# Performance work log

Hardware: AMD Instinct MI355X
Metric: run time of the kernel (lower is better)

Reference implementation:

```python
import jax, jax.numpy as jnp
import numpy as np

B, C, H, W = 4, 256, 64, 64
D, K = 256, 32
EPS = 1e-12  # F.normalize clamp

def setup_inputs() -> dict:
    key = jax.random.key(0)
    k1, k2, k3, k4 = jax.random.split(key, 4)
    x = jax.random.normal(k1, (B, C, H, W), dtype=jnp.float32)
    w_theta = jax.random.normal(k2, (D, C), dtype=jnp.float32) * 0.05  # 1x1 conv theta
    w_phi = jax.random.normal(k3, (K, C // K), dtype=jnp.float32) * 0.1  # grouped 1x1 conv phi
    scale = jax.random.uniform(k4, (D, K), dtype=jnp.float32, minval=-1.0, maxval=0.0)
    return {"x": x, "w_theta": w_theta, "w_phi": w_phi, "scale": scale}

def reference(x, w_theta, w_phi, scale):
    b, c, h, w = x.shape
    d, k = scale.shape
    n = h * w
    xf = x.reshape(b, c, n)                                   # B,D,N (C==D)
    # --- Gen_code ---
    xg = xf.reshape(b, k, c // k, n)                          # grouped 1x1 conv
    x_phi = jnp.einsum('bkcn,kc->bnk', xg, w_phi)             # B,N,K
    x_phi = jax.nn.softmax(x_phi, axis=1)                     # softmax over pixels
    x_theta = jnp.einsum('dc,bcn->bdn', w_theta, xf)          # B,D,N
    code = jnp.einsum('bdn,bnk->bdk', x_theta, x_phi)         # B,D,K
    code = code / jnp.maximum(jnp.linalg.norm(code, axis=1, keepdims=True), EPS)
    # (dropout p=0.15 treated as identity)
    # --- embedded residual, without materializing B,N,D,K ---
    s2 = scale * scale                                        # D,K
    t1 = jnp.einsum('bdn,dk->bnk', xf * xf, s2)
    t2 = jnp.einsum('bdn,bdk->bnk', xf, s2[None] * code)
    t3 = jnp.einsum('dk,bdk->bk', s2, code * code)
    dist = t1 - 2.0 * t2 + t3[:, None, :]                     # sum_d (scale*(x-code))^2
    Q = jax.nn.softmax(-0.5 * dist, axis=2)                   # B,N,K
    Qsum = Q.sum(axis=1)                                      # B,K
    # Z_[b,d,k] = sum_n Q*residual / Qsum = scale*(sum_n Q x / Qsum - code)
    Z_ = scale[None] * (jnp.einsum('bdn,bnk->bdk', xf, Q) / Qsum[:, None, :] - code)
    Z = Z_ / jnp.sqrt((Z_ * Z_).sum(axis=1, keepdims=True))   # torch sqrt, no eps
    return Z, Q
```

## Files before the change

### kernel.cpp

```cpp
#include <hip/hip_runtime.h>
#include <math.h>

#define BB 4
#define CC 256
#define NN 4096
#define KK 32
#define DD 256
#define GG 8
#define NT2 64
#define NE 8

__device__ __forceinline__ float wredsum(float v) {
#pragma unroll
  for (int o = 32; o > 0; o >>= 1) v += __shfl_xor(v, o, 64);
  return v;
}

__global__ __launch_bounds__(256) void k_phi(const float* __restrict__ x,
                                             const float* __restrict__ wphi,
                                             float* __restrict__ phi,
                                             float* __restrict__ Sp) {
  const int half = blockIdx.x & 1;
  const int k = (blockIdx.x >> 1) & 31;
  const int b = blockIdx.x >> 6;
  const int tid = threadIdx.x;
  const float* xb = x + (size_t)(b * CC + k * GG) * NN + half * 2048;
  float w[GG];
#pragma unroll
  for (int j = 0; j < GG; ++j) w[j] = wphi[k * GG + j];
  float4 v[2];
  float sum = 0.f;
#pragma unroll
  for (int i = 0; i < 2; ++i) {
    const int n = i * 1024 + tid * 4;
    float4 s = make_float4(0.f, 0.f, 0.f, 0.f);
#pragma unroll
    for (int j = 0; j < GG; ++j) {
      const float4 xv = *reinterpret_cast<const float4*>(xb + (size_t)j * NN + n);
      s.x = fmaf(xv.x, w[j], s.x);
      s.y = fmaf(xv.y, w[j], s.y);
      s.z = fmaf(xv.z, w[j], s.z);
      s.w = fmaf(xv.w, w[j], s.w);
    }
    v[i].x = __expf(s.x);
    v[i].y = __expf(s.y);
    v[i].z = __expf(s.z);
    v[i].w = __expf(s.w);
    sum += v[i].x + v[i].y + v[i].z + v[i].w;
  }
  float* pk = phi + (size_t)(b * KK + k) * NN + half * 2048;
#pragma unroll
  for (int i = 0; i < 2; ++i) {
    *reinterpret_cast<float4*>(pk + i * 1024 + tid * 4) = v[i];
  }
  __shared__ float rb[4];
  sum = wredsum(sum);
  if ((tid & 63) == 0) rb[tid >> 6] = sum;
  __syncthreads();
  if (tid == 0)
    Sp[((size_t)half * BB + b) * KK + k] = rb[0] + rb[1] + rb[2] + rb[3];
}

__global__ __launch_bounds__(256) void k_xpT(const float* __restrict__ x,
                                             const float* __restrict__ phi,
                                             float* __restrict__ m1e) {
  const int e = blockIdx.x & 7;
  const int ct = (blockIdx.x >> 3) & 31;
  const int b = blockIdx.x >> 8;
  const int tid = threadIdx.x;
  __shared__ float smem[256 * 33];
  const int kl = tid >> 3;
  const int nq = tid & 7;
  const int k = tid & 31;
  const int g = tid >> 5;
  const float* xb = x + (size_t)(b * CC + ct * 8) * NN + e * 512;
  float acc[8] = {0.f, 0.f, 0.f, 0.f, 0.f, 0.f, 0.f, 0.f};
#pragma unroll
  for (int ch = 0; ch < 2; ++ch) {
    const float* pch = phi + (size_t)(b * KK + kl) * NN + e * 512 + ch * 256;
#pragma unroll
    for (int j = 0; j < 8; ++j) {
      const int nn = (j * 8 + nq) * 4;
      const float4 pv = *reinterpret_cast<const float4*>(pch + nn);
      smem[(nn + 0) * 33 + kl] = pv.x;
      smem[(nn + 1) * 33 + kl] = pv.y;
      smem[(nn + 2) * 33 + kl] = pv.z;
      smem[(nn + 3) * 33 + kl] = pv.w;
    }
    __syncthreads();
#pragma unroll
    for (int i = 0; i < 8; ++i) {
      const int nl = g * 32 + i * 4;
      const float p0 = smem[(nl + 0) * 33 + k];
      const float p1 = smem[(nl + 1) * 33 + k];
      const float p2 = smem[(nl + 2) * 33 + k];
      const float p3 = smem[(nl + 3) * 33 + k];
#pragma unroll
      for (int c = 0; c < 8; ++c) {
        const float4 xv =
            *reinterpret_cast<const float4*>(xb + (size_t)c * NN + ch * 256 + nl);
        acc[c] = fmaf(xv.x, p0, acc[c]);
        acc[c] = fmaf(xv.y, p1, acc[c]);
        acc[c] = fmaf(xv.z, p2, acc[c]);
        acc[c] = fmaf(xv.w, p3, acc[c]);
      }
    }
    __syncthreads();
  }
#pragma unroll
  for (int c = 0; c < 8; ++c) smem[(g * 8 + c) * 33 + k] = acc[c];
  __syncthreads();
  const int c2 = tid & 7, k2 = tid >> 3;
  float s = 0.f;
#pragma unroll
  for (int gg = 0; gg < 8; ++gg) s += smem[(gg * 8 + c2) * 33 + k2];
  m1e[((size_t)(e * BB + b) * KK + k2) * CC + ct * 8 + c2] = s;
}

__global__ __launch_bounds__(256) void k_code(const float* __restrict__ m1e,
                                              const float* __restrict__ Sp,
                                              const float* __restrict__ wth,
                                              const float* __restrict__ scale,
                                              float* __restrict__ code,
                                              float* __restrict__ bc2,
                                              float* __restrict__ s2g,
                                              float* __restrict__ t3) {
  const int b = blockIdx.x >> 5;
  const int k = blockIdx.x & 31;
  const int d = threadIdx.x;
  const float invS =
      1.f / (Sp[(size_t)b * KK + k] + Sp[((size_t)BB + b) * KK + k]);
  __shared__ __align__(16) float m1s[CC];
  float m = 0.f;
#pragma unroll
  for (int e = 0; e < NE; ++e)
    m += m1e[((size_t)(e * BB + b) * KK + k) * CC + d];
  m1s[d] = m * invS;
  __syncthreads();
  float cd = 0.f;
  const float* wt = wth + (size_t)d * CC;
#pragma unroll 4
  for (int c = 0; c < CC; c += 4) {
    const float4 w4 = *reinterpret_cast<const float4*>(wt + c);
    const float4 m4 = *reinterpret_cast<const float4*>(&m1s[c]);
    cd = fmaf(w4.x, m4.x, cd);
    cd = fmaf(w4.y, m4.y, cd);
    cd = fmaf(w4.z, m4.z, cd);
    cd = fmaf(w4.w, m4.w, cd);
  }
  __shared__ float rb[4];
  float ss = wredsum(cd * cd);
  if ((d & 63) == 0) rb[d >> 6] = ss;
  __syncthreads();
  const float nrm = sqrtf(rb[0] + rb[1] + rb[2] + rb[3]);
  const float inv = 1.f / fmaxf(nrm, 1e-12f);
  cd *= inv;
  const float sc = scale[(size_t)d * KK + k];
  const float s2 = sc * sc;
  code[((size_t)b * DD + d) * KK + k] = cd;
  bc2[((size_t)b * DD + d) * KK + k] = 2.f * s2 * cd;
  if (b == 0) s2g[(size_t)d * KK + k] = s2;
  float tt = wredsum(s2 * cd * cd);
  __syncthreads();
  if ((d & 63) == 0) rb[d >> 6] = tt;
  __syncthreads();
  if (d == 0) t3[b * KK + k] = rb[0] + rb[1] + rb[2] + rb[3];
}

__global__ __launch_bounds__(512) void k_dist(const float* __restrict__ x,
                                              const float* __restrict__ s2g,
                                              const float* __restrict__ bc2,
                                              const float* __restrict__ t3,
                                              float* __restrict__ qout,
                                              float* __restrict__ qpart) {
  const int b = blockIdx.x >> 6;
  const int tile = blockIdx.x & 63;
  const int n0 = tile * 64;
  const int tid = threadIdx.x;
  const int lane = tid & 63;
  const int wid = __builtin_amdgcn_readfirstlane(tid >> 6);
  const int d0 = wid * 32;
  __shared__ float lds[4 * 64 * 33];
  __shared__ float smax[64 * 9];
  __shared__ float ssum[64 * 9];
  float accA[32], accB[32];
#pragma unroll
  for (int k = 0; k < 32; ++k) { accA[k] = 0.f; accB[k] = 0.f; }
  const float* xb = x + ((size_t)b * CC + d0) * NN + n0 + lane;
  const float* s2b = s2g + (size_t)d0 * KK;
  const float* bcb = bc2 + ((size_t)b * DD + d0) * KK;
#pragma unroll 2
  for (int dd = 0; dd < 32; ++dd) {
    const float xv = xb[(size_t)dd * NN];
    const float x2 = xv * xv;
    const float* s2r = s2b + dd * KK;
    const float* bcr = bcb + dd * KK;
#pragma unroll
    for (int k = 0; k < 32; ++k) {
      accA[k] = fmaf(x2, s2r[k], accA[k]);
      accB[k] = fmaf(xv, bcr[k], accB[k]);
    }
  }
  if (wid >= 4) {
    float* Lp = lds + ((size_t)((wid - 4) * 64 + lane)) * 33;
#pragma unroll
    for (int k = 0; k < 32; ++k) Lp[k] = accA[k] - accB[k];
  }
  __syncthreads();
  if (wid < 4) {
    float* Lp = lds + ((size_t)(wid * 64 + lane)) * 33;
#pragma unroll
    for (int k = 0; k < 32; ++k) Lp[k] += accA[k] - accB[k];
  }
  __syncthreads();
  const int n = lane;
  const int kq = wid;
  float vals[4];
#pragma unroll
  for (int j = 0; j < 4; ++j) {
    const int k = kq * 4 + j;
    float s = 0.f;
#pragma unroll
    for (int g = 0; g < 4; ++g) s += lds[((size_t)(g * 64 + n)) * 33 + k];
    vals[j] = -0.5f * (s + t3[b * KK + k]);
  }
  float m4 = fmaxf(fmaxf(vals[0], vals[1]), fmaxf(vals[2], vals[3]));
  smax[n * 9 + kq] = m4;
  __syncthreads();
  float m = smax[n * 9 + 0];
#pragma unroll
  for (int g = 1; g < 8; ++g) m = fmaxf(m, smax[n * 9 + g]);
  float e[4];
  float ps = 0.f;
#pragma unroll
  for (int j = 0; j < 4; ++j) {
    e[j] = __expf(vals[j] - m);
    ps += e[j];
  }
  ssum[n * 9 + kq] = ps;
  __syncthreads();
  float tot = 0.f;
#pragma unroll
  for (int g = 0; g < 8; ++g) tot += ssum[n * 9 + g];
  const float inv = 1.f / tot;
  float4 q4;
  q4.x = e[0] * inv; q4.y = e[1] * inv; q4.z = e[2] * inv; q4.w = e[3] * inv;
  *reinterpret_cast<float4*>(qout + ((size_t)b * NN + n0 + n) * KK + kq * 4) = q4;
  float qs[4] = {q4.x, q4.y, q4.z, q4.w};
#pragma unroll
  for (int j = 0; j < 4; ++j) {
    const float v = wredsum(qs[j]);
    if (n == 0) qpart[((size_t)b * KK + kq * 4 + j) * NT2 + tile] = v;
  }
}

__global__ __launch_bounds__(256) void k_xq(const float* __restrict__ x,
                                            const float* __restrict__ q,
                                            float* __restrict__ znq8) {
  const int e = blockIdx.x & 7;
  const int ct = (blockIdx.x >> 3) & 31;
  const int b = blockIdx.x >> 8;
  const int tid = threadIdx.x;
  const int k = tid & 31;
  const int g = tid >> 5;
  const int n0 = e * 512 + g * 64;
  const float* xb = x + (size_t)(b * CC + ct * 8) * NN;
  const float* qb = q + (size_t)b * NN * KK + k;
  float acc[8] = {0.f, 0.f, 0.f, 0.f, 0.f, 0.f, 0.f, 0.f};
  for (int n = n0; n < n0 + 64; n += 4) {
    const float p0 = qb[(size_t)(n + 0) * KK];
    const float p1 = qb[(size_t)(n + 1) * KK];
    const float p2 = qb[(size_t)(n + 2) * KK];
    const float p3 = qb[(size_t)(n + 3) * KK];
#pragma unroll
    for (int c = 0; c < 8; ++c) {
      const float4 xv = *reinterpret_cast<const float4*>(xb + (size_t)c * NN + n);
      acc[c] = fmaf(xv.x, p0, acc[c]);
      acc[c] = fmaf(xv.y, p1, acc[c]);
      acc[c] = fmaf(xv.z, p2, acc[c]);
      acc[c] = fmaf(xv.w, p3, acc[c]);
    }
  }
  __shared__ float lds[8 * 8 * 33];
#pragma unroll
  for (int c = 0; c < 8; ++c) lds[(g * 8 + c) * 33 + k] = acc[c];
  __syncthreads();
  const int c2 = tid & 7, k2 = tid >> 3;
  float s = 0.f;
#pragma unroll
  for (int gg = 0; gg < 8; ++gg) s += lds[(gg * 8 + c2) * 33 + k2];
  znq8[((size_t)(e * BB + b) * KK + k2) * CC + ct * 8 + c2] = s;
}

__global__ __launch_bounds__(256) void k_z(const float* __restrict__ znq8,
                                           const float* __restrict__ code,
                                           const float* __restrict__ scale,
                                           const float* __restrict__ qpart,
                                           float* __restrict__ zout) {
  const int b = blockIdx.x >> 5;
  const int k = blockIdx.x & 31;
  const int d = threadIdx.x;
  __shared__ float rb[4];
  float qp = 0.f;
  if (d < NT2) qp = qpart[((size_t)b * KK + k) * NT2 + d];
  qp = wredsum(qp);
  if ((d & 63) == 0) rb[d >> 6] = qp;
  __syncthreads();
  const float qs = rb[0] + rb[1] + rb[2] + rb[3];
  float zn = 0.f;
#pragma unroll
  for (int e = 0; e < NE; ++e)
    zn += znq8[((size_t)(e * BB + b) * KK + k) * CC + d];
  const float cd = code[((size_t)b * DD + d) * KK + k];
  const float z_ = scale[(size_t)d * KK + k] * (zn / qs - cd);
  float ss = wredsum(z_ * z_);
  __syncthreads();
  if ((d & 63) == 0) rb[d >> 6] = ss;
  __syncthreads();
  const float rn = 1.f / sqrtf(rb[0] + rb[1] + rb[2] + rb[3]);
  zout[((size_t)b * DD + d) * KK + k] = z_ * rn;
}

extern "C" void kernel_launch(void* const* d_in, const int* in_sizes, int n_in,
                              void* d_out, int out_size, void* d_ws, size_t ws_size,
                              hipStream_t stream) {
  const float* x = (const float*)d_in[0];
  const float* wth = (const float*)d_in[1];
  const float* wphi = (const float*)d_in[2];
  const float* scale = (const float*)d_in[3];
  float* out = (float*)d_out;
  float* zout = out;
  float* qout = out + (size_t)BB * DD * KK;
  float* ws = (float*)d_ws;
  float* phi = ws;
  float* Sp = phi + (size_t)BB * NN * KK;
  float* m1e = Sp + 2 * (size_t)BB * KK;
  float* code = m1e + (size_t)NE * BB * KK * CC;
  float* bc2 = code + (size_t)BB * DD * KK;
  float* s2g = bc2 + (size_t)BB * DD * KK;
  float* t3 = s2g + (size_t)DD * KK;
  float* qpart = t3 + BB * KK;
  float* znq8 = qpart + (size_t)BB * KK * NT2;

  k_phi<<<BB * KK * 2, 256, 0, stream>>>(x, wphi, phi, Sp);
  k_xpT<<<BB * 32 * NE, 256, 0, stream>>>(x, phi, m1e);
  k_code<<<BB * KK, 256, 0, stream>>>(m1e, Sp, wth, scale, code, bc2, s2g, t3);
  k_dist<<<BB * NT2, 512, 0, stream>>>(x, s2g, bc2, t3, qout, qpart);
  k_xq<<<BB * 32 * NE, 256, 0, stream>>>(x, qout, znq8);
  k_z<<<BB * KK, 256, 0, stream>>>(znq8, code, scale, qpart, zout);
}
```

Measured before the change: 78.03 us.

## Fuse six kernels into one cooperative kernel with grid-wide syncs

```diff
diff --git a/kernel.cpp b/kernel.cpp
--- a/kernel.cpp
+++ b/kernel.cpp
@@ -1,5 +1,8 @@
 #include <hip/hip_runtime.h>
+#include <hip/hip_cooperative_groups.h>
 #include <math.h>
+
+namespace cg = cooperative_groups;
 
 #define BB 4
 #define CC 256
@@ -16,314 +19,356 @@
   return v;
 }
 
-__global__ __launch_bounds__(256) void k_phi(const float* __restrict__ x,
-                                             const float* __restrict__ wphi,
-                                             float* __restrict__ phi,
-                                             float* __restrict__ Sp) {
-  const int half = blockIdx.x & 1;
-  const int k = (blockIdx.x >> 1) & 31;
-  const int b = blockIdx.x >> 6;
+__global__ __launch_bounds__(512) void k_mega(
+    const float* __restrict__ x, const float* __restrict__ wth,
+    const float* __restrict__ wphi, const float* __restrict__ scale,
+    float* __restrict__ zout, float* __restrict__ qout,
+    float* __restrict__ phi, float* __restrict__ Sp, float* __restrict__ m1e,
+    float* __restrict__ code, float* __restrict__ bc2, float* __restrict__ s2g,
+    float* __restrict__ t3, float* __restrict__ qpart,
+    float* __restrict__ znq8) {
+  cg::grid_group grid = cg::this_grid();
+  const int bid = blockIdx.x;
   const int tid = threadIdx.x;
-  const float* xb = x + (size_t)(b * CC + k * GG) * NN + half * 2048;
-  float w[GG];
-#pragma unroll
-  for (int j = 0; j < GG; ++j) w[j] = wphi[k * GG + j];
-  float4 v[2];
-  float sum = 0.f;
-#pragma unroll
-  for (int i = 0; i < 2; ++i) {
-    const int n = i * 1024 + tid * 4;
+  __shared__ float smem[9600];
+  __shared__ float rb[8];
+
+  {
+    const int half = bid & 1, k = (bid >> 1) & 31, b = bid >> 6;
+    const int n = half * 2048 + tid * 4;
+    const float* xb = x + (size_t)(b * CC + k * GG) * NN + n;
+    float w[GG];
+#pragma unroll
+    for (int j = 0; j < GG; ++j) w[j] = wphi[k * GG + j];
     float4 s = make_float4(0.f, 0.f, 0.f, 0.f);
 #pragma unroll
     for (int j = 0; j < GG; ++j) {
-      const float4 xv = *reinterpret_cast<const float4*>(xb + (size_t)j * NN + n);
+      const float4 xv = *reinterpret_cast<const float4*>(xb + (size_t)j * NN);
       s.x = fmaf(xv.x, w[j], s.x);
       s.y = fmaf(xv.y, w[j], s.y);
       s.z = fmaf(xv.z, w[j], s.z);
       s.w = fmaf(xv.w, w[j], s.w);
     }
-    v[i].x = __expf(s.x);
-    v[i].y = __expf(s.y);
-    v[i].z = __expf(s.z);
-    v[i].w = __expf(s.w);
-    sum += v[i].x + v[i].y + v[i].z + v[i].w;
-  }
-  float* pk = phi + (size_t)(b * KK + k) * NN + half * 2048;
-#pragma unroll
-  for (int i = 0; i < 2; ++i) {
-    *reinterpret_cast<float4*>(pk + i * 1024 + tid * 4) = v[i];
-  }
-  __shared__ float rb[4];
-  sum = wredsum(sum);
-  if ((tid & 63) == 0) rb[tid >> 6] = sum;
-  __syncthreads();
-  if (tid == 0)
-    Sp[((size_t)half * BB + b) * KK + k] = rb[0] + rb[1] + rb[2] + rb[3];
+    float4 e4;
+    e4.x = __expf(s.x); e4.y = __expf(s.y);
+    e4.z = __expf(s.z); e4.w = __expf(s.w);
+    *reinterpret_cast<float4*>(phi + (size_t)(b * KK + k) * NN + n) = e4;
+    float sum = wredsum(e4.x + e4.y + e4.z + e4.w);
+    if ((tid & 63) == 0) rb[tid >> 6] = sum;
+    __syncthreads();
+    if (tid == 0) {
+      float t = 0.f;
+#pragma unroll
+      for (int i = 0; i < 8; ++i) t += rb[i];
+      Sp[((size_t)half * BB + b) * KK + k] = t;
+    }
+  }
+  grid.sync();
+
+  {
+    const int b = bid >> 6, e = (bid >> 3) & 7, ct = bid & 7;
+    const int k = tid & 31, g = tid >> 5;
+    const int kl = tid >> 4, nq = tid & 15;
+    float acc[32];
+#pragma unroll
+    for (int c = 0; c < 32; ++c) acc[c] = 0.f;
+    const int ne0 = e * 512;
+    const float* xbase = x + (size_t)(b * CC + ct * 32) * NN;
+#pragma unroll
+    for (int ch = 0; ch < 2; ++ch) {
+      const int n0 = ne0 + ch * 256;
+      const float* pk = phi + (size_t)(b * KK + kl) * NN + n0 + nq * 16;
+#pragma unroll
+      for (int j = 0; j < 4; ++j) {
+        const float4 pv = *reinterpret_cast<const float4*>(pk + j * 4);
+        const int nn = nq * 16 + j * 4;
+        smem[(nn + 0) * 33 + kl] = pv.x;
+        smem[(nn + 1) * 33 + kl] = pv.y;
+        smem[(nn + 2) * 33 + kl] = pv.z;
+        smem[(nn + 3) * 33 + kl] = pv.w;
+      }
+      __syncthreads();
+      float ph[16];
+#pragma unroll
+      for (int i = 0; i < 16; ++i) ph[i] = smem[(g * 16 + i) * 33 + k];
+#pragma unroll
+      for (int c = 0; c < 32; ++c) {
+        const float* xr = xbase + (size_t)c * NN + n0 + g * 16;
+#pragma unroll
+        for (int j = 0; j < 4; ++j) {
+          const float4 xv = *reinterpret_cast<const float4*>(xr + j * 4);
+          acc[c] = fmaf(xv.x, ph[j * 4 + 0], acc[c]);
+          acc[c] = fmaf(xv.y, ph[j * 4 + 1], acc[c]);
+          acc[c] = fmaf(xv.z, ph[j * 4 + 2], acc[c]);
+          acc[c] = fmaf(xv.w, ph[j * 4 + 3], acc[c]);
+        }
+      }
+      __syncthreads();
+    }
+    if (g >= 8) {
+#pragma unroll
+      for (int c = 0; c < 32; ++c) smem[((g - 8) * 32 + c) * 33 + k] = acc[c];
+    }
+    __syncthreads();
+    if (g < 8) {
+#pragma unroll
+      for (int c = 0; c < 32; ++c) smem[(g * 32 + c) * 33 + k] += acc[c];
+    }
+    __syncthreads();
+#pragma unroll
+    for (int o = 0; o < 2; ++o) {
+      const int idx = o * 512 + tid;
+      const int c2 = idx >> 5, k2 = idx & 31;
+      float s = 0.f;
+#pragma unroll
+      for (int gg = 0; gg < 8; ++gg) s += smem[(gg * 32 + c2) * 33 + k2];
+      m1e[((size_t)(e * BB + b) * KK + k2) * CC + ct * 32 + c2] = s;
+    }
+  }
+  grid.sync();
+
+  {
+    const bool blkact = bid < 128;
+    const int b = (bid >> 5) & 3, k = bid & 31;
+    const bool act = blkact && (tid < 256);
+    const int d = tid;
+    if (act) {
+      const float invS =
+          1.f / (Sp[(size_t)b * KK + k] + Sp[((size_t)BB + b) * KK + k]);
+      float m = 0.f;
+#pragma unroll
+      for (int e = 0; e < NE; ++e)
+        m += m1e[((size_t)(e * BB + b) * KK + k) * CC + d];
+      smem[d] = m * invS;
+    }
+    __syncthreads();
+    float cd = 0.f;
+    if (act) {
+      const float* wt = wth + (size_t)d * CC;
+#pragma unroll 4
+      for (int c = 0; c < CC; c += 4) {
+        const float4 w4 = *reinterpret_cast<const float4*>(wt + c);
+        cd = fmaf(w4.x, smem[c + 0], cd);
+        cd = fmaf(w4.y, smem[c + 1], cd);
+        cd = fmaf(w4.z, smem[c + 2], cd);
+        cd = fmaf(w4.w, smem[c + 3], cd);
+      }
+    }
+    float ss = wredsum(act ? cd * cd : 0.f);
+    if ((tid & 63) == 0) rb[tid >> 6] = ss;
+    __syncthreads();
+    float nr2 = 0.f;
+#pragma unroll
+    for (int i = 0; i < 8; ++i) nr2 += rb[i];
+    const float inv = 1.f / fmaxf(sqrtf(nr2), 1e-12f);
+    float tt = 0.f;
+    if (act) {
+      cd *= inv;
+      const float sc = scale[(size_t)d * KK + k];
+      const float s2 = sc * sc;
+      code[((size_t)b * DD + d) * KK + k] = cd;
+      bc2[((size_t)b * DD + d) * KK + k] = 2.f * s2 * cd;
+      if (b == 0) s2g[(size_t)d * KK + k] = s2;
+      tt = s2 * cd * cd;
+    }
+    float t2 = wredsum(tt);
+    __syncthreads();
+    if ((tid & 63) == 0) rb[tid >> 6] = t2;
+    __syncthreads();
+    if (blkact && tid == 0) {
+      float t = 0.f;
+#pragma unroll
+      for (int i = 0; i < 8; ++i) t += rb[i];
+      t3[b * KK + k] = t;
+    }
+  }
+  grid.sync();
+
+  {
+    float* lds = smem;
+    float* smax = smem + 8448;
+    float* ssum = smem + 9024;
+    const int b = bid >> 6;
+    const int tile = bid & 63;
+    const int n0 = tile * 64;
+    const int lane = tid & 63;
+    const int wid = __builtin_amdgcn_readfirstlane(tid >> 6);
+    const int d0 = wid * 32;
+    float accA[32], accB[32];
+#pragma unroll
+    for (int k = 0; k < 32; ++k) { accA[k] = 0.f; accB[k] = 0.f; }
+    const float* xb = x + ((size_t)b * CC + d0) * NN + n0 + lane;
+    const float* s2b = s2g + (size_t)d0 * KK;
+    const float* bcb = bc2 + ((size_t)b * DD + d0) * KK;
+#pragma unroll 2
+    for (int dd = 0; dd < 32; ++dd) {
+      const float xv = xb[(size_t)dd * NN];
+      const float x2 = xv * xv;
+      const float* s2r = s2b + dd * KK;
+      const float* bcr = bcb + dd * KK;
+#pragma unroll
+      for (int k = 0; k < 32; ++k) {
+        accA[k] = fmaf(x2, s2r[k], accA[k]);
+        accB[k] = fmaf(xv, bcr[k], accB[k]);
+      }
+    }
+    if (wid >= 4) {
+      float* Lp = lds + ((size_t)((wid - 4) * 64 + lane)) * 33;
+#pragma unroll
+      for (int k = 0; k < 32; ++k) Lp[k] = accA[k] - accB[k];
+    }
+    __syncthreads();
+    if (wid < 4) {
+      float* Lp = lds + ((size_t)(wid * 64 + lane)) * 33;
+#pragma unroll
+      for (int k = 0; k < 32; ++k) Lp[k] += accA[k] - accB[k];
+    }
+    __syncthreads();
+    const int n = lane;
+    const int kq = wid;
+    float vals[4];
+#pragma unroll
+    for (int j = 0; j < 4; ++j) {
+      const int k = kq * 4 + j;
+      float s = 0.f;
+#pragma unroll
+      for (int g = 0; g < 4; ++g) s += lds[((size_t)(g * 64 + n)) * 33 + k];
+      vals[j] = -0.5f * (s + t3[b * KK + k]);
+    }
+    float m4 = fmaxf(fmaxf(vals[0], vals[1]), fmaxf(vals[2], vals[3]));
+    smax[n * 9 + kq] = m4;
+    __syncthreads();
+    float m = smax[n * 9 + 0];
+#pragma unroll
+    for (int g = 1; g < 8; ++g) m = fmaxf(m, smax[n * 9 + g]);
+    float e[4];
+    float ps = 0.f;
+#pragma unroll
+    for (int j = 0; j < 4; ++j) {
+      e[j] = __expf(vals[j] - m);
+      ps += e[j];
+    }
+    ssum[n * 9 + kq] = ps;
+    __syncthreads();
+    float tot = 0.f;
+#pragma unroll
+    for (int g = 0; g < 8; ++g) tot += ssum[n * 9 + g];
+    const float inv = 1.f / tot;
+    float4 q4;
+    q4.x = e[0] * inv; q4.y = e[1] * inv;
+    q4.z = e[2] * inv; q4.w = e[3] * inv;
+    *reinterpret_cast<float4*>(qout + ((size_t)b * NN + n0 + n) * KK + kq * 4) =
+        q4;
+    float qs[4] = {q4.x, q4.y, q4.z, q4.w};
+#pragma unroll
+    for (int j = 0; j < 4; ++j) {
+      const float v = wredsum(qs[j]);
+      if (n == 0) qpart[((size_t)b * KK + kq * 4 + j) * NT2 + tile] = v;
+    }
+  }
+  grid.sync();
+
+  {
+    const int b = bid >> 6, e = (bid >> 3) & 7, ct = bid & 7;
+    const int k = tid & 31, g = tid >> 5;
+    float acc[32];
+#pragma unroll
+    for (int c = 0; c < 32; ++c) acc[c] = 0.f;
+    const int ne0 = e * 512;
+    const float* xbase = x + (size_t)(b * CC + ct * 32) * NN;
+#pragma unroll
+    for (int ch = 0; ch < 2; ++ch) {
+      const int n0 = ne0 + ch * 256;
+      const int r = tid >> 1, ko = (tid & 1) * 16;
+      const float* qr = qout + ((size_t)b * NN + n0 + r) * KK + ko;
+#pragma unroll
+      for (int j = 0; j < 4; ++j) {
+        const float4 qv = *reinterpret_cast<const float4*>(qr + j * 4);
+        const int kk = ko + j * 4;
+        smem[r * 33 + kk + 0] = qv.x;
+        smem[r * 33 + kk + 1] = qv.y;
+        smem[r * 33 + kk + 2] = qv.z;
+        smem[r * 33 + kk + 3] = qv.w;
+      }
+      __syncthreads();
+      float ph[16];
+#pragma unroll
+      for (int i = 0; i < 16; ++i) ph[i] = smem[(g * 16 + i) * 33 + k];
+#pragma unroll
+      for (int c = 0; c < 32; ++c) {
+        const float* xr = xbase + (size_t)c * NN + n0 + g * 16;
+#pragma unroll
+        for (int j = 0; j < 4; ++j) {
+          const float4 xv = *reinterpret_cast<const float4*>(xr + j * 4);
+          acc[c] = fmaf(xv.x, ph[j * 4 + 0], acc[c]);
+          acc[c] = fmaf(xv.y, ph[j * 4 + 1], acc[c]);
+          acc[c] = fmaf(xv.z, ph[j * 4 + 2], acc[c]);
+          acc[c] = fmaf(xv.w, ph[j * 4 + 3], acc[c]);
+        }
+      }
+      __syncthreads();
+    }
+    if (g >= 8) {
+#pragma unroll
+      for (int c = 0; c < 32; ++c) smem[((g - 8) * 32 + c) * 33 + k] = acc[c];
+    }
+    __syncthreads();
+    if (g < 8) {
+#pragma unroll
+      for (int c = 0; c < 32; ++c) smem[(g * 32 + c) * 33 + k] += acc[c];
+    }
+    __syncthreads();
+#pragma unroll
+    for (int o = 0; o < 2; ++o) {
+      const int idx = o * 512 + tid;
+      const int c2 = idx >> 5, k2 = idx & 31;
+      float s = 0.f;
+#pragma unroll
+      for (int gg = 0; gg < 8; ++gg) s += smem[(gg * 32 + c2) * 33 + k2];
+      znq8[((size_t)(e * BB + b) * KK + k2) * CC + ct * 32 + c2] = s;
+    }
+  }
+  grid.sync();
+
+  {
+    const bool blkact = bid < 128;
+    const int b = (bid >> 5) & 3, k = bid & 31;
+    const bool act = blkact && (tid < 256);
+    const int d = tid;
+    float qp = (blkact && tid < NT2)
+                   ? qpart[((size_t)b * KK + k) * NT2 + tid]
+                   : 0.f;
+    float qpw = wredsum(qp);
+    if ((tid & 63) == 0) rb[tid >> 6] = qpw;
+    __syncthreads();
+    float qs = 0.f;
+#pragma unroll
+    for (int i = 0; i < 8; ++i) qs += rb[i];
+    float z_ = 0.f;
+    if (act) {
+      float zn = 0.f;
+#pragma unroll
+      for (int e = 0; e < NE; ++e)
+        zn += znq8[((size_t)(e * BB + b) * KK + k) * CC + d];
+      const float cdv = code[((size_t)b * DD + d) * KK + k];
+      z_ = scale[(size_t)d * KK + k] * (zn / qs - cdv);
+    }
+    float ss = wredsum(act ? z_ * z_ : 0.f);
+    __syncthreads();
+    if ((tid & 63) == 0) rb[tid >> 6] = ss;
+    __syncthreads();
+    if (act) {
+      float t = 0.f;
+#pragma unroll
+      for (int i = 0; i < 8; ++i) t += rb[i];
+      zout[((size_t)b * DD + d) * KK + k] = z_ * (1.f / sqrtf(t));
+    }
+  }
 }
 
-__global__ __launch_bounds__(256) void k_xpT(const float* __restrict__ x,
-                                             const float* __restrict__ phi,
-                                             float* __restrict__ m1e) {
-  const int e = blockIdx.x & 7;
-  const int ct = (blockIdx.x >> 3) & 31;
-  const int b = blockIdx.x >> 8;
-  const int tid = threadIdx.x;
-  __shared__ float smem[256 * 33];
-  const int kl = tid >> 3;
-  const int nq = tid & 7;
-  const int k = tid & 31;
-  const int g = tid >> 5;
-  const float* xb = x + (size_t)(b * CC + ct * 8) * NN + e * 512;
-  float acc[8] = {0.f, 0.f, 0.f, 0.f, 0.f, 0.f, 0.f, 0.f};
-#pragma unroll
-  for (int ch = 0; ch < 2; ++ch) {
-    const float* pch = phi + (size_t)(b * KK + kl) * NN + e * 512 + ch * 256;
-#pragma unroll
-    for (int j = 0; j < 8; ++j) {
-      const int nn = (j * 8 + nq) * 4;
-      const float4 pv = *reinterpret_cast<const float4*>(pch + nn);
-      smem[(nn + 0) * 33 + kl] = pv.x;
-      smem[(nn + 1) * 33 + kl] = pv.y;
-      smem[(nn + 2) * 33 + kl] = pv.z;
-      smem[(nn + 3) * 33 + kl] = pv.w;
-    }
-    __syncthreads();
-#pragma unroll
-    for (int i = 0; i < 8; ++i) {
-      const int nl = g * 32 + i * 4;
-      const float p0 = smem[(nl + 0) * 33 + k];
-      const float p1 = smem[(nl + 1) * 33 + k];
-      const float p2 = smem[(nl + 2) * 33 + k];
-      const float p3 = smem[(nl + 3) * 33 + k];
-#pragma unroll
-      for (int c = 0; c < 8; ++c) {
-        const float4 xv =
-            *reinterpret_cast<const float4*>(xb + (size_t)c * NN + ch * 256 + nl);
-        acc[c] = fmaf(xv.x, p0, acc[c]);
-        acc[c] = fmaf(xv.y, p1, acc[c]);
-        acc[c] = fmaf(xv.z, p2, acc[c]);
-        acc[c] = fmaf(xv.w, p3, acc[c]);
-      }
-    }
-    __syncthreads();
-  }
-#pragma unroll
-  for (int c = 0; c < 8; ++c) smem[(g * 8 + c) * 33 + k] = acc[c];
-  __syncthreads();
-  const int c2 = tid & 7, k2 = tid >> 3;
-  float s = 0.f;
-#pragma unroll
-  for (int gg = 0; gg < 8; ++gg) s += smem[(gg * 8 + c2) * 33 + k2];
-  m1e[((size_t)(e * BB + b) * KK + k2) * CC + ct * 8 + c2] = s;
-}
-
-__global__ __launch_bounds__(256) void k_code(const float* __restrict__ m1e,
-                                              const float* __restrict__ Sp,
-                                              const float* __restrict__ wth,
-                                              const float* __restrict__ scale,
-                                              float* __restrict__ code,
-                                              float* __restrict__ bc2,
-                                              float* __restrict__ s2g,
-                                              float* __restrict__ t3) {
-  const int b = blockIdx.x >> 5;
-  const int k = blockIdx.x & 31;
-  const int d = threadIdx.x;
-  const float invS =
-      1.f / (Sp[(size_t)b * KK + k] + Sp[((size_t)BB + b) * KK + k]);
-  __shared__ __align__(16) float m1s[CC];
-  float m = 0.f;
-#pragma unroll
-  for (int e = 0; e < NE; ++e)
-    m += m1e[((size_t)(e * BB + b) * KK + k) * CC + d];
-  m1s[d] = m * invS;
-  __syncthreads();
-  float cd = 0.f;
-  const float* wt = wth + (size_t)d * CC;
-#pragma unroll 4
-  for (int c = 0; c < CC; c += 4) {
-    const float4 w4 = *reinterpret_cast<const float4*>(wt + c);
-    const float4 m4 = *reinterpret_cast<const float4*>(&m1s[c]);
-    cd = fmaf(w4.x, m4.x, cd);
-    cd = fmaf(w4.y, m4.y, cd);
-    cd = fmaf(w4.z, m4.z, cd);
-    cd = fmaf(w4.w, m4.w, cd);
-  }
-  __shared__ float rb[4];
-  float ss = wredsum(cd * cd);
-  if ((d & 63) == 0) rb[d >> 6] = ss;
-  __syncthreads();
-  const float nrm = sqrtf(rb[0] + rb[1] + rb[2] + rb[3]);
-  const float inv = 1.f / fmaxf(nrm, 1e-12f);
-  cd *= inv;
-  const float sc = scale[(size_t)d * KK + k];
-  const float s2 = sc * sc;
-  code[((size_t)b * DD + d) * KK + k] = cd;
-  bc2[((size_t)b * DD + d) * KK + k] = 2.f * s2 * cd;
-  if (b == 0) s2g[(size_t)d * KK + k] = s2;
-  float tt = wredsum(s2 * cd * cd);
-  __syncthreads();
-  if ((d & 63) == 0) rb[d >> 6] = tt;
-  __syncthreads();
-  if (d == 0) t3[b * KK + k] = rb[0] + rb[1] + rb[2] + rb[3];
-}
-
-__global__ __launch_bounds__(512) void k_dist(const float* __restrict__ x,
-                                              const float* __restrict__ s2g,
-                                              const float* __restrict__ bc2,
-                                              const float* __restrict__ t3,
-                                              float* __restrict__ qout,
-                                              float* __restrict__ qpart) {
-  const int b = blockIdx.x >> 6;
-  const int tile = blockIdx.x & 63;
-  const int n0 = tile * 64;
-  const int tid = threadIdx.x;
-  const int lane = tid & 63;
-  const int wid = __builtin_amdgcn_readfirstlane(tid >> 6);
-  const int d0 = wid * 32;
-  __shared__ float lds[4 * 64 * 33];
-  __shared__ float smax[64 * 9];
-  __shared__ float ssum[64 * 9];
-  float accA[32], accB[32];
-#pragma unroll
-  for (int k = 0; k < 32; ++k) { accA[k] = 0.f; accB[k] = 0.f; }
-  const float* xb = x + ((size_t)b * CC + d0) * NN + n0 + lane;
-  const float* s2b = s2g + (size_t)d0 * KK;
-  const float* bcb = bc2 + ((size_t)b * DD + d0) * KK;
-#pragma unroll 2
-  for (int dd = 0; dd < 32; ++dd) {
-    const float xv = xb[(size_t)dd * NN];
-    const float x2 = xv * xv;
-    const float* s2r = s2b + dd * KK;
-    const float* bcr = bcb + dd * KK;
-#pragma unroll
-    for (int k = 0; k < 32; ++k) {
-      accA[k] = fmaf(x2, s2r[k], accA[k]);
-      accB[k] = fmaf(xv, bcr[k], accB[k]);
-    }
-  }
-  if (wid >= 4) {
-    float* Lp = lds + ((size_t)((wid - 4) * 64 + lane)) * 33;
-#pragma unroll
-    for (int k = 0; k < 32; ++k) Lp[k] = accA[k] - accB[k];
-  }
-  __syncthreads();
-  if (wid < 4) {
-    float* Lp = lds + ((size_t)(wid * 64 + lane)) * 33;
-#pragma unroll
-    for (int k = 0; k < 32; ++k) Lp[k] += accA[k] - accB[k];
-  }
-  __syncthreads();
-  const int n = lane;
-  const int kq = wid;
-  float vals[4];
-#pragma unroll
-  for (int j = 0; j < 4; ++j) {
-    const int k = kq * 4 + j;
-    float s = 0.f;
-#pragma unroll
-    for (int g = 0; g < 4; ++g) s += lds[((size_t)(g * 64 + n)) * 33 + k];
-    vals[j] = -0.5f * (s + t3[b * KK + k]);
-  }
-  float m4 = fmaxf(fmaxf(vals[0], vals[1]), fmaxf(vals[2], vals[3]));
-  smax[n * 9 + kq] = m4;
-  __syncthreads();
-  float m = smax[n * 9 + 0];
-#pragma unroll
-  for (int g = 1; g < 8; ++g) m = fmaxf(m, smax[n * 9 + g]);
-  float e[4];
-  float ps = 0.f;
-#pragma unroll
-  for (int j = 0; j < 4; ++j) {
-    e[j] = __expf(vals[j] - m);
-    ps += e[j];
-  }
-  ssum[n * 9 + kq] = ps;
-  __syncthreads();
-  float tot = 0.f;
-#pragma unroll
-  for (int g = 0; g < 8; ++g) tot += ssum[n * 9 + g];
-  const float inv = 1.f / tot;
-  float4 q4;
-  q4.x = e[0] * inv; q4.y = e[1] * inv; q4.z = e[2] * inv; q4.w = e[3] * inv;
-  *reinterpret_cast<float4*>(qout + ((size_t)b * NN + n0 + n) * KK + kq * 4) = q4;
-  float qs[4] = {q4.x, q4.y, q4.z, q4.w};
-#pragma unroll
-  for (int j = 0; j < 4; ++j) {
-    const float v = wredsum(qs[j]);
-    if (n == 0) qpart[((size_t)b * KK + kq * 4 + j) * NT2 + tile] = v;
-  }
-}
-
-__global__ __launch_bounds__(256) void k_xq(const float* __restrict__ x,
-                                            const float* __restrict__ q,
-                                            float* __restrict__ znq8) {
-  const int e = blockIdx.x & 7;
-  const int ct = (blockIdx.x >> 3) & 31;
-  const int b = blockIdx.x >> 8;
-  const int tid = threadIdx.x;
-  const int k = tid & 31;
-  const int g = tid >> 5;
-  const int n0 = e * 512 + g * 64;
-  const float* xb = x + (size_t)(b * CC + ct * 8) * NN;
-  const float* qb = q + (size_t)b * NN * KK + k;
-  float acc[8] = {0.f, 0.f, 0.f, 0.f, 0.f, 0.f, 0.f, 0.f};
-  for (int n = n0; n < n0 + 64; n += 4) {
-    const float p0 = qb[(size_t)(n + 0) * KK];
-    const float p1 = qb[(size_t)(n + 1) * KK];
-    const float p2 = qb[(size_t)(n + 2) * KK];
-    const float p3 = qb[(size_t)(n + 3) * KK];
-#pragma unroll
-    for (int c = 0; c < 8; ++c) {
-      const float4 xv = *reinterpret_cast<const float4*>(xb + (size_t)c * NN + n);
-      acc[c] = fmaf(xv.x, p0, acc[c]);
-      acc[c] = fmaf(xv.y, p1, acc[c]);
-      acc[c] = fmaf(xv.z, p2, acc[c]);
-      acc[c] = fmaf(xv.w, p3, acc[c]);
-    }
-  }
-  __shared__ float lds[8 * 8 * 33];
-#pragma unroll
-  for (int c = 0; c < 8; ++c) lds[(g * 8 + c) * 33 + k] = acc[c];
-  __syncthreads();
-  const int c2 = tid & 7, k2 = tid >> 3;
-  float s = 0.f;
-#pragma unroll
-  for (int gg = 0; gg < 8; ++gg) s += lds[(gg * 8 + c2) * 33 + k2];
-  znq8[((size_t)(e * BB + b) * KK + k2) * CC + ct * 8 + c2] = s;
-}
-
-__global__ __launch_bounds__(256) void k_z(const float* __restrict__ znq8,
-                                           const float* __restrict__ code,
-                                           const float* __restrict__ scale,
-                                           const float* __restrict__ qpart,
-                                           float* __restrict__ zout) {
-  const int b = blockIdx.x >> 5;
-  const int k = blockIdx.x & 31;
-  const int d = threadIdx.x;
-  __shared__ float rb[4];
-  float qp = 0.f;
-  if (d < NT2) qp = qpart[((size_t)b * KK + k) * NT2 + d];
-  qp = wredsum(qp);
-  if ((d & 63) == 0) rb[d >> 6] = qp;
-  __syncthreads();
-  const float qs = rb[0] + rb[1] + rb[2] + rb[3];
-  float zn = 0.f;
-#pragma unroll
-  for (int e = 0; e < NE; ++e)
-    zn += znq8[((size_t)(e * BB + b) * KK + k) * CC + d];
-  const float cd = code[((size_t)b * DD + d) * KK + k];
-  const float z_ = scale[(size_t)d * KK + k] * (zn / qs - cd);
-  float ss = wredsum(z_ * z_);
-  __syncthreads();
-  if ((d & 63) == 0) rb[d >> 6] = ss;
-  __syncthreads();
-  const float rn = 1.f / sqrtf(rb[0] + rb[1] + rb[2] + rb[3]);
-  zout[((size_t)b * DD + d) * KK + k] = z_ * rn;
-}
-
 extern "C" void kernel_launch(void* const* d_in, const int* in_sizes, int n_in,
-                              void* d_out, int out_size, void* d_ws, size_t ws_size,
-                              hipStream_t stream) {
+                              void* d_out, int out_size, void* d_ws,
+                              size_t ws_size, hipStream_t stream) {
   const float* x = (const float*)d_in[0];
   const float* wth = (const float*)d_in[1];
   const float* wphi = (const float*)d_in[2];
@@ -342,10 +387,8 @@
   float* qpart = t3 + BB * KK;
   float* znq8 = qpart + (size_t)BB * KK * NT2;
 
-  k_phi<<<BB * KK * 2, 256, 0, stream>>>(x, wphi, phi, Sp);
-  k_xpT<<<BB * 32 * NE, 256, 0, stream>>>(x, phi, m1e);
-  k_code<<<BB * KK, 256, 0, stream>>>(m1e, Sp, wth, scale, code, bc2, s2g, t3);
-  k_dist<<<BB * NT2, 512, 0, stream>>>(x, s2g, bc2, t3, qout, qpart);
-  k_xq<<<BB * 32 * NE, 256, 0, stream>>>(x, qout, znq8);
-  k_z<<<BB * KK, 256, 0, stream>>>(znq8, code, scale, qpart, zout);
+  void* args[] = {&x,    &wth, &wphi, &scale, &zout, &qout, &phi,  &Sp,
+                  &m1e,  &code, &bc2,  &s2g,   &t3,   &qpart, &znq8};
+  hipLaunchCooperativeKernel((const void*)k_mega, dim3(256), dim3(512), args,
+                             0, stream);
 }
```

Result: slower. 259.6 us (+232.6%).

## Fuse phi generation into x·phi reduction and x·Q into distance kernel

Applied to the files above, without the earlier changes.

```diff
diff --git a/kernel.cpp b/kernel.cpp
--- a/kernel.cpp
+++ b/kernel.cpp
@@ -7,8 +7,7 @@
 #define KK 32
 #define DD 256
 #define GG 8
-#define NT2 64
-#define NE 8
+#define NEs 64
 
 __device__ __forceinline__ float wredsum(float v) {
 #pragma unroll
@@ -16,109 +15,83 @@
   return v;
 }
 
-__global__ __launch_bounds__(256) void k_phi(const float* __restrict__ x,
+__global__ __launch_bounds__(512) void k_pm1(const float* __restrict__ x,
                                              const float* __restrict__ wphi,
-                                             float* __restrict__ phi,
-                                             float* __restrict__ Sp) {
-  const int half = blockIdx.x & 1;
-  const int k = (blockIdx.x >> 1) & 31;
+                                             float* __restrict__ m1e,
+                                             float* __restrict__ SpE) {
   const int b = blockIdx.x >> 6;
+  const int e = blockIdx.x & 63;
+  const int n0 = e * 64;
   const int tid = threadIdx.x;
-  const float* xb = x + (size_t)(b * CC + k * GG) * NN + half * 2048;
-  float w[GG];
-#pragma unroll
-  for (int j = 0; j < GG; ++j) w[j] = wphi[k * GG + j];
-  float4 v[2];
-  float sum = 0.f;
-#pragma unroll
-  for (int i = 0; i < 2; ++i) {
-    const int n = i * 1024 + tid * 4;
+  __shared__ float phis[32 * 65];
+  __shared__ float tr[256 * 33];
+  {
+    const int kk = tid >> 4;
+    const int m = tid & 15;
+    const float* xb = x + (size_t)(b * CC + kk * GG) * NN + n0 + m * 4;
+    float w[GG];
+#pragma unroll
+    for (int j = 0; j < GG; ++j) w[j] = wphi[kk * GG + j];
     float4 s = make_float4(0.f, 0.f, 0.f, 0.f);
 #pragma unroll
     for (int j = 0; j < GG; ++j) {
-      const float4 xv = *reinterpret_cast<const float4*>(xb + (size_t)j * NN + n);
+      const float4 xv = *reinterpret_cast<const float4*>(xb + (size_t)j * NN);
       s.x = fmaf(xv.x, w[j], s.x);
       s.y = fmaf(xv.y, w[j], s.y);
       s.z = fmaf(xv.z, w[j], s.z);
       s.w = fmaf(xv.w, w[j], s.w);
     }
-    v[i].x = __expf(s.x);
-    v[i].y = __expf(s.y);
-    v[i].z = __expf(s.z);
-    v[i].w = __expf(s.w);
-    sum += v[i].x + v[i].y + v[i].z + v[i].w;
-  }
-  float* pk = phi + (size_t)(b * KK + k) * NN + half * 2048;
-#pragma unroll
-  for (int i = 0; i < 2; ++i) {
-    *reinterpret_cast<float4*>(pk + i * 1024 + tid * 4) = v[i];
-  }
-  __shared__ float rb[4];
-  sum = wredsum(sum);
-  if ((tid & 63) == 0) rb[tid >> 6] = sum;
-  __syncthreads();
-  if (tid == 0)
-    Sp[((size_t)half * BB + b) * KK + k] = rb[0] + rb[1] + rb[2] + rb[3];
-}
-
-__global__ __launch_bounds__(256) void k_xpT(const float* __restrict__ x,
-                                             const float* __restrict__ phi,
-                                             float* __restrict__ m1e) {
-  const int e = blockIdx.x & 7;
-  const int ct = (blockIdx.x >> 3) & 31;
-  const int b = blockIdx.x >> 8;
-  const int tid = threadIdx.x;
-  __shared__ float smem[256 * 33];
-  const int kl = tid >> 3;
-  const int nq = tid & 7;
+    float* pr = phis + kk * 65 + m * 4;
+    pr[0] = __expf(s.x);
+    pr[1] = __expf(s.y);
+    pr[2] = __expf(s.z);
+    pr[3] = __expf(s.w);
+  }
+  __syncthreads();
+  if (tid < 32) {
+    float s = 0.f;
+#pragma unroll 8
+    for (int n = 0; n < 64; ++n) s += phis[tid * 65 + n];
+    SpE[((size_t)e * BB + b) * KK + tid] = s;
+  }
   const int k = tid & 31;
-  const int g = tid >> 5;
-  const float* xb = x + (size_t)(b * CC + ct * 8) * NN + e * 512;
-  float acc[8] = {0.f, 0.f, 0.f, 0.f, 0.f, 0.f, 0.f, 0.f};
-#pragma unroll
-  for (int ch = 0; ch < 2; ++ch) {
-    const float* pch = phi + (size_t)(b * KK + kl) * NN + e * 512 + ch * 256;
-#pragma unroll
-    for (int j = 0; j < 8; ++j) {
-      const int nn = (j * 8 + nq) * 4;
-      const float4 pv = *reinterpret_cast<const float4*>(pch + nn);
-      smem[(nn + 0) * 33 + kl] = pv.x;
-      smem[(nn + 1) * 33 + kl] = pv.y;
-      smem[(nn + 2) * 33 + kl] = pv.z;
-      smem[(nn + 3) * 33 + kl] = pv.w;
-    }
-    __syncthreads();
-#pragma unroll
-    for (int i = 0; i < 8; ++i) {
-      const int nl = g * 32 + i * 4;
-      const float p0 = smem[(nl + 0) * 33 + k];
-      const float p1 = smem[(nl + 1) * 33 + k];
-      const float p2 = smem[(nl + 2) * 33 + k];
-      const float p3 = smem[(nl + 3) * 33 + k];
-#pragma unroll
-      for (int c = 0; c < 8; ++c) {
-        const float4 xv =
-            *reinterpret_cast<const float4*>(xb + (size_t)c * NN + ch * 256 + nl);
-        acc[c] = fmaf(xv.x, p0, acc[c]);
-        acc[c] = fmaf(xv.y, p1, acc[c]);
-        acc[c] = fmaf(xv.z, p2, acc[c]);
-        acc[c] = fmaf(xv.w, p3, acc[c]);
+  const int ct = tid >> 5;
+  float acc[16];
+#pragma unroll
+  for (int c = 0; c < 16; ++c) acc[c] = 0.f;
+  const float* xm = x + (size_t)(b * CC + ct * 16) * NN + n0;
+#pragma unroll
+  for (int sub = 0; sub < 4; ++sub) {
+    float ph[16];
+#pragma unroll
+    for (int i = 0; i < 16; ++i) ph[i] = phis[k * 65 + sub * 16 + i];
+#pragma unroll
+    for (int c = 0; c < 16; ++c) {
+      const float* xr = xm + (size_t)c * NN + sub * 16;
+#pragma unroll
+      for (int n4 = 0; n4 < 4; ++n4) {
+        const float4 xv = *reinterpret_cast<const float4*>(xr + n4 * 4);
+        acc[c] = fmaf(xv.x, ph[n4 * 4 + 0], acc[c]);
+        acc[c] = fmaf(xv.y, ph[n4 * 4 + 1], acc[c]);
+        acc[c] = fmaf(xv.z, ph[n4 * 4 + 2], acc[c]);
+        acc[c] = fmaf(xv.w, ph[n4 * 4 + 3], acc[c]);
       }
     }
-    __syncthreads();
-  }
-#pragma unroll
-  for (int c = 0; c < 8; ++c) smem[(g * 8 + c) * 33 + k] = acc[c];
-  __syncthreads();
-  const int c2 = tid & 7, k2 = tid >> 3;
-  float s = 0.f;
-#pragma unroll
-  for (int gg = 0; gg < 8; ++gg) s += smem[(gg * 8 + c2) * 33 + k2];
-  m1e[((size_t)(e * BB + b) * KK + k2) * CC + ct * 8 + c2] = s;
+  }
+#pragma unroll
+  for (int i = 0; i < 16; ++i) tr[(ct * 16 + i) * 33 + k] = acc[i];
+  __syncthreads();
+  float* mb = m1e + ((size_t)e * BB + b) * KK * CC;
+#pragma unroll
+  for (int o = 0; o < 16; ++o) {
+    const int idx = o * 512 + tid;
+    const int c2 = idx & 255, k2 = idx >> 8;
+    mb[(size_t)k2 * CC + c2] = tr[c2 * 33 + k2];
+  }
 }
 
 __global__ __launch_bounds__(256) void k_code(const float* __restrict__ m1e,
-                                              const float* __restrict__ Sp,
+                                              const float* __restrict__ SpE,
                                               const float* __restrict__ wth,
                                               const float* __restrict__ scale,
                                               float* __restrict__ code,
@@ -128,13 +101,16 @@
   const int b = blockIdx.x >> 5;
   const int k = blockIdx.x & 31;
   const int d = threadIdx.x;
-  const float invS =
-      1.f / (Sp[(size_t)b * KK + k] + Sp[((size_t)BB + b) * KK + k]);
   __shared__ __align__(16) float m1s[CC];
+  __shared__ float rb[4];
+  float sp = (d < NEs) ? SpE[((size_t)d * BB + b) * KK + k] : 0.f;
+  sp = wredsum(sp);
+  if ((d & 63) == 0) rb[d >> 6] = sp;
+  __syncthreads();
+  const float invS = 1.f / (rb[0] + rb[1] + rb[2] + rb[3]);
   float m = 0.f;
-#pragma unroll
-  for (int e = 0; e < NE; ++e)
-    m += m1e[((size_t)(e * BB + b) * KK + k) * CC + d];
+  for (int e = 0; e < NEs; ++e)
+    m += m1e[(((size_t)e * BB + b) * KK + k) * CC + d];
   m1s[d] = m * invS;
   __syncthreads();
   float cd = 0.f;
@@ -148,8 +124,8 @@
     cd = fmaf(w4.z, m4.z, cd);
     cd = fmaf(w4.w, m4.w, cd);
   }
-  __shared__ float rb[4];
   float ss = wredsum(cd * cd);
+  __syncthreads();
   if ((d & 63) == 0) rb[d >> 6] = ss;
   __syncthreads();
   const float nrm = sqrtf(rb[0] + rb[1] + rb[2] + rb[3]);
@@ -167,12 +143,13 @@
   if (d == 0) t3[b * KK + k] = rb[0] + rb[1] + rb[2] + rb[3];
 }
 
-__global__ __launch_bounds__(512) void k_dist(const float* __restrict__ x,
-                                              const float* __restrict__ s2g,
-                                              const float* __restrict__ bc2,
-                                              const float* __restrict__ t3,
-                                              float* __restrict__ qout,
-                                              float* __restrict__ qpart) {
+__global__ __launch_bounds__(512) void k_distq(const float* __restrict__ x,
+                                               const float* __restrict__ s2g,
+                                               const float* __restrict__ bc2,
+                                               const float* __restrict__ t3,
+                                               float* __restrict__ qout,
+                                               float* __restrict__ qpart,
+                                               float* __restrict__ znt) {
   const int b = blockIdx.x >> 6;
   const int tile = blockIdx.x & 63;
   const int n0 = tile * 64;
@@ -183,22 +160,25 @@
   __shared__ float lds[4 * 64 * 33];
   __shared__ float smax[64 * 9];
   __shared__ float ssum[64 * 9];
+  __shared__ float qlds[64 * 33];
   float accA[32], accB[32];
 #pragma unroll
   for (int k = 0; k < 32; ++k) { accA[k] = 0.f; accB[k] = 0.f; }
-  const float* xb = x + ((size_t)b * CC + d0) * NN + n0 + lane;
-  const float* s2b = s2g + (size_t)d0 * KK;
-  const float* bcb = bc2 + ((size_t)b * DD + d0) * KK;
+  {
+    const float* xb = x + ((size_t)b * CC + d0) * NN + n0 + lane;
+    const float* s2b = s2g + (size_t)d0 * KK;
+    const float* bcb = bc2 + ((size_t)b * DD + d0) * KK;
 #pragma unroll 2
-  for (int dd = 0; dd < 32; ++dd) {
-    const float xv = xb[(size_t)dd * NN];
-    const float x2 = xv * xv;
-    const float* s2r = s2b + dd * KK;
-    const float* bcr = bcb + dd * KK;
-#pragma unroll
-    for (int k = 0; k < 32; ++k) {
-      accA[k] = fmaf(x2, s2r[k], accA[k]);
-      accB[k] = fmaf(xv, bcr[k], accB[k]);
+    for (int dd = 0; dd < 32; ++dd) {
+      const float xv = xb[(size_t)dd * NN];
+      const float x2 = xv * xv;
+      const float* s2r = s2b + dd * KK;
+      const float* bcr = bcb + dd * KK;
+#pragma unroll
+      for (int k = 0; k < 32; ++k) {
+        accA[k] = fmaf(x2, s2r[k], accA[k]);
+        accB[k] = fmaf(xv, bcr[k], accB[k]);
+      }
     }
   }
   if (wid >= 4) {
@@ -213,86 +193,91 @@
     for (int k = 0; k < 32; ++k) Lp[k] += accA[k] - accB[k];
   }
   __syncthreads();
-  const int n = lane;
-  const int kq = wid;
-  float vals[4];
-#pragma unroll
-  for (int j = 0; j < 4; ++j) {
-    const int k = kq * 4 + j;
-    float s = 0.f;
-#pragma unroll
-    for (int g = 0; g < 4; ++g) s += lds[((size_t)(g * 64 + n)) * 33 + k];
-    vals[j] = -0.5f * (s + t3[b * KK + k]);
-  }
-  float m4 = fmaxf(fmaxf(vals[0], vals[1]), fmaxf(vals[2], vals[3]));
-  smax[n * 9 + kq] = m4;
-  __syncthreads();
-  float m = smax[n * 9 + 0];
-#pragma unroll
-  for (int g = 1; g < 8; ++g) m = fmaxf(m, smax[n * 9 + g]);
-  float e[4];
-  float ps = 0.f;
-#pragma unroll
-  for (int j = 0; j < 4; ++j) {
-    e[j] = __expf(vals[j] - m);
-    ps += e[j];
-  }
-  ssum[n * 9 + kq] = ps;
-  __syncthreads();
-  float tot = 0.f;
-#pragma unroll
-  for (int g = 0; g < 8; ++g) tot += ssum[n * 9 + g];
-  const float inv = 1.f / tot;
-  float4 q4;
-  q4.x = e[0] * inv; q4.y = e[1] * inv; q4.z = e[2] * inv; q4.w = e[3] * inv;
-  *reinterpret_cast<float4*>(qout + ((size_t)b * NN + n0 + n) * KK + kq * 4) = q4;
-  float qs[4] = {q4.x, q4.y, q4.z, q4.w};
-#pragma unroll
-  for (int j = 0; j < 4; ++j) {
-    const float v = wredsum(qs[j]);
-    if (n == 0) qpart[((size_t)b * KK + kq * 4 + j) * NT2 + tile] = v;
-  }
-}
-
-__global__ __launch_bounds__(256) void k_xq(const float* __restrict__ x,
-                                            const float* __restrict__ q,
-                                            float* __restrict__ znq8) {
-  const int e = blockIdx.x & 7;
-  const int ct = (blockIdx.x >> 3) & 31;
-  const int b = blockIdx.x >> 8;
-  const int tid = threadIdx.x;
-  const int k = tid & 31;
-  const int g = tid >> 5;
-  const int n0 = e * 512 + g * 64;
-  const float* xb = x + (size_t)(b * CC + ct * 8) * NN;
-  const float* qb = q + (size_t)b * NN * KK + k;
-  float acc[8] = {0.f, 0.f, 0.f, 0.f, 0.f, 0.f, 0.f, 0.f};
-  for (int n = n0; n < n0 + 64; n += 4) {
-    const float p0 = qb[(size_t)(n + 0) * KK];
-    const float p1 = qb[(size_t)(n + 1) * KK];
-    const float p2 = qb[(size_t)(n + 2) * KK];
-    const float p3 = qb[(size_t)(n + 3) * KK];
-#pragma unroll
-    for (int c = 0; c < 8; ++c) {
-      const float4 xv = *reinterpret_cast<const float4*>(xb + (size_t)c * NN + n);
-      acc[c] = fmaf(xv.x, p0, acc[c]);
-      acc[c] = fmaf(xv.y, p1, acc[c]);
-      acc[c] = fmaf(xv.z, p2, acc[c]);
-      acc[c] = fmaf(xv.w, p3, acc[c]);
-    }
-  }
-  __shared__ float lds[8 * 8 * 33];
-#pragma unroll
-  for (int c = 0; c < 8; ++c) lds[(g * 8 + c) * 33 + k] = acc[c];
-  __syncthreads();
-  const int c2 = tid & 7, k2 = tid >> 3;
-  float s = 0.f;
-#pragma unroll
-  for (int gg = 0; gg < 8; ++gg) s += lds[(gg * 8 + c2) * 33 + k2];
-  znq8[((size_t)(e * BB + b) * KK + k2) * CC + ct * 8 + c2] = s;
-}
-
-__global__ __launch_bounds__(256) void k_z(const float* __restrict__ znq8,
+  {
+    const int n = lane;
+    const int kq = wid;
+    float vals[4];
+#pragma unroll
+    for (int j = 0; j < 4; ++j) {
+      const int k = kq * 4 + j;
+      float s = 0.f;
+#pragma unroll
+      for (int g = 0; g < 4; ++g) s += lds[((size_t)(g * 64 + n)) * 33 + k];
+      vals[j] = -0.5f * (s + t3[b * KK + k]);
+    }
+    float m4 = fmaxf(fmaxf(vals[0], vals[1]), fmaxf(vals[2], vals[3]));
+    smax[n * 9 + kq] = m4;
+    __syncthreads();
+    float m = smax[n * 9 + 0];
+#pragma unroll
+    for (int g = 1; g < 8; ++g) m = fmaxf(m, smax[n * 9 + g]);
+    float e[4];
+    float ps = 0.f;
+#pragma unroll
+    for (int j = 0; j < 4; ++j) {
+      e[j] = __expf(vals[j] - m);
+      ps += e[j];
+    }
+    ssum[n * 9 + kq] = ps;
+    __syncthreads();
+    float tot = 0.f;
+#pragma unroll
+    for (int g = 0; g < 8; ++g) tot += ssum[n * 9 + g];
+    const float inv = 1.f / tot;
+    float4 q4;
+    q4.x = e[0] * inv; q4.y = e[1] * inv;
+    q4.z = e[2] * inv; q4.w = e[3] * inv;
+    *reinterpret_cast<float4*>(qout + ((size_t)b * NN + n0 + n) * KK + kq * 4) =
+        q4;
+    float* qr = qlds + n * 33 + kq * 4;
+    qr[0] = q4.x; qr[1] = q4.y; qr[2] = q4.z; qr[3] = q4.w;
+    float qs[4] = {q4.x, q4.y, q4.z, q4.w};
+#pragma unroll
+    for (int j = 0; j < 4; ++j) {
+      const float v = wredsum(qs[j]);
+      if (n == 0) qpart[((size_t)b * KK + kq * 4 + j) * NEs + tile] = v;
+    }
+  }
+  __syncthreads();
+  {
+    const int k = tid & 31;
+    const int ct = tid >> 5;
+    float acc[16];
+#pragma unroll
+    for (int c = 0; c < 16; ++c) acc[c] = 0.f;
+    const float* xq = x + (size_t)(b * CC + ct * 16) * NN + n0;
+#pragma unroll
+    for (int sub = 0; sub < 4; ++sub) {
+      float qq[16];
+#pragma unroll
+      for (int i = 0; i < 16; ++i) qq[i] = qlds[(sub * 16 + i) * 33 + k];
+#pragma unroll
+      for (int c = 0; c < 16; ++c) {
+        const float* xr = xq + (size_t)c * NN + sub * 16;
+#pragma unroll
+        for (int n4 = 0; n4 < 4; ++n4) {
+          const float4 xv = *reinterpret_cast<const float4*>(xr + n4 * 4);
+          acc[c] = fmaf(xv.x, qq[n4 * 4 + 0], acc[c]);
+          acc[c] = fmaf(xv.y, qq[n4 * 4 + 1], acc[c]);
+          acc[c] = fmaf(xv.z, qq[n4 * 4 + 2], acc[c]);
+          acc[c] = fmaf(xv.w, qq[n4 * 4 + 3], acc[c]);
+        }
+      }
+    }
+#pragma unroll
+    for (int i = 0; i < 16; ++i) lds[(ct * 16 + i) * 33 + k] = acc[i];
+    __syncthreads();
+    float* zb = znt + ((size_t)b * NEs + tile) * KK * CC;
+#pragma unroll
+    for (int o = 0; o < 16; ++o) {
+      const int idx = o * 512 + tid;
+      const int c2 = idx & 255, k2 = idx >> 8;
+      zb[(size_t)k2 * CC + c2] = lds[c2 * 33 + k2];
+    }
+  }
+}
+
+__global__ __launch_bounds__(256) void k_z(const float* __restrict__ znt,
                                            const float* __restrict__ code,
                                            const float* __restrict__ scale,
                                            const float* __restrict__ qpart,
@@ -301,16 +286,21 @@
   const int k = blockIdx.x & 31;
   const int d = threadIdx.x;
   __shared__ float rb[4];
-  float qp = 0.f;
-  if (d < NT2) qp = qpart[((size_t)b * KK + k) * NT2 + d];
+  float qp = (d < NEs) ? qpart[((size_t)b * KK + k) * NEs + d] : 0.f;
   qp = wredsum(qp);
   if ((d & 63) == 0) rb[d >> 6] = qp;
   __syncthreads();
   const float qs = rb[0] + rb[1] + rb[2] + rb[3];
-  float zn = 0.f;
-#pragma unroll
-  for (int e = 0; e < NE; ++e)
-    zn += znq8[((size_t)(e * BB + b) * KK + k) * CC + d];
+  const float* zp = znt + ((size_t)b * NEs * KK + k) * CC + d;
+  float z0 = 0.f, z1 = 0.f, z2 = 0.f, z3 = 0.f;
+  const size_t tstr = (size_t)KK * CC;
+  for (int t = 0; t < NEs; t += 4) {
+    z0 += zp[(size_t)(t + 0) * tstr];
+    z1 += zp[(size_t)(t + 1) * tstr];
+    z2 += zp[(size_t)(t + 2) * tstr];
+    z3 += zp[(size_t)(t + 3) * tstr];
+  }
+  const float zn = (z0 + z1) + (z2 + z3);
   const float cd = code[((size_t)b * DD + d) * KK + k];
   const float z_ = scale[(size_t)d * KK + k] * (zn / qs - cd);
   float ss = wredsum(z_ * z_);
@@ -322,8 +312,8 @@
 }
 
 extern "C" void kernel_launch(void* const* d_in, const int* in_sizes, int n_in,
-                              void* d_out, int out_size, void* d_ws, size_t ws_size,
-                              hipStream_t stream) {
+                              void* d_out, int out_size, void* d_ws,
+                              size_t ws_size, hipStream_t stream) {
   const float* x = (const float*)d_in[0];
   const float* wth = (const float*)d_in[1];
   const float* wphi = (const float*)d_in[2];
@@ -332,20 +322,17 @@
   float* zout = out;
   float* qout = out + (size_t)BB * DD * KK;
   float* ws = (float*)d_ws;
-  float* phi = ws;
-  float* Sp = phi + (size_t)BB * NN * KK;
-  float* m1e = Sp + 2 * (size_t)BB * KK;
-  float* code = m1e + (size_t)NE * BB * KK * CC;
+  float* SpE = ws;
+  float* m1e = SpE + (size_t)NEs * BB * KK;
+  float* code = m1e + (size_t)NEs * BB * KK * CC;
   float* bc2 = code + (size_t)BB * DD * KK;
   float* s2g = bc2 + (size_t)BB * DD * KK;
   float* t3 = s2g + (size_t)DD * KK;
   float* qpart = t3 + BB * KK;
-  float* znq8 = qpart + (size_t)BB * KK * NT2;
-
-  k_phi<<<BB * KK * 2, 256, 0, stream>>>(x, wphi, phi, Sp);
-  k_xpT<<<BB * 32 * NE, 256, 0, stream>>>(x, phi, m1e);
-  k_code<<<BB * KK, 256, 0, stream>>>(m1e, Sp, wth, scale, code, bc2, s2g, t3);
-  k_dist<<<BB * NT2, 512, 0, stream>>>(x, s2g, bc2, t3, qout, qpart);
-  k_xq<<<BB * 32 * NE, 256, 0, stream>>>(x, qout, znq8);
-  k_z<<<BB * KK, 256, 0, stream>>>(znq8, code, scale, qpart, zout);
-}
+  float* znt = qpart + (size_t)BB * KK * NEs;
+
+  k_pm1<<<BB * NEs, 512, 0, stream>>>(x, wphi, m1e, SpE);
+  k_code<<<BB * KK, 256, 0, stream>>>(m1e, SpE, wth, scale, code, bc2, s2g, t3);
+  k_distq<<<BB * NEs, 512, 0, stream>>>(x, s2g, bc2, t3, qout, qpart, znt);
+  k_z<<<BB * KK, 256, 0, stream>>>(znt, code, scale, qpart, zout);
+}
```

Result: slower. 91.85 us (+17.7%).
